# Kernel optimization log

Hardware: AMD Instinct MI355X
Metric: run time of the kernel (lower is better)

Reference implementation:

```python
import jax, jax.numpy as jnp
import numpy as np

D_MODEL = 256
N_HEADS = 8
D_HEAD = D_MODEL // N_HEADS
EMB = [16, 16, 16, 16]
CUMSUM = [0, 16, 32, 48, 64]
PSUM = sum(EMB)
LEVELS = [(122, 122), (61, 61), (31, 31), (16, 16)]
S_TOTAL = sum(h * w for h, w in LEVELS)
IMG = 976.0


def swap_pairs(x):
    # swap consecutive pairs along the leading (view) dim
    return x.reshape(-1, 2, *x.shape[1:])[:, ::-1].reshape(x.shape)


def grid_sample_bilinear(img, grid):
    # img: [B, H, W, D]; grid: [B, Q, 2] in [-1, 1]; align_corners=False, zero padding
    B, H, W, D = img.shape
    gx = (grid[..., 0] + 1.0) * (W * 0.5) - 0.5
    gy = (grid[..., 1] + 1.0) * (H * 0.5) - 0.5
    x0 = jnp.floor(gx)
    y0 = jnp.floor(gy)
    wx = (gx - x0)[..., None]
    wy = (gy - y0)[..., None]
    x0i = x0.astype(jnp.int32)
    y0i = y0.astype(jnp.int32)
    flat = img.reshape(B, H * W, D)

    def gather(xi, yi):
        valid = ((xi >= 0) & (xi < W) & (yi >= 0) & (yi < H)).astype(img.dtype)
        idx = jnp.clip(yi, 0, H - 1) * W + jnp.clip(xi, 0, W - 1)
        v = jnp.take_along_axis(flat, idx[..., None], axis=1)
        return v * valid[..., None]

    v00 = gather(x0i, y0i)
    v01 = gather(x0i + 1, y0i)
    v10 = gather(x0i, y0i + 1)
    v11 = gather(x0i + 1, y0i + 1)
    return (v00 * (1 - wx) * (1 - wy) + v01 * wx * (1 - wy)
            + v10 * (1 - wx) * wy + v11 * wx * wy)


def ms_deform_attn_core(value, shapes, sampling_locations, attention_weights):
    # value: [N, S, M, D]; sampling_locations: [N, Lq, M, P, 2]; attention_weights: [N, Lq, M, P]
    N, S, M, D = value.shape
    Lq = sampling_locations.shape[1]
    grids = 2.0 * sampling_locations - 1.0
    outs = []
    start = 0
    for lid, (H, W) in enumerate(shapes):
        p0, p1 = CUMSUM[lid], CUMSUM[lid + 1]
        Pl = p1 - p0
        v = value[:, start:start + H * W].reshape(N, H, W, M, D)
        v = v.transpose(0, 3, 1, 2, 4).reshape(N * M, H, W, D)
        g = grids[:, :, :, p0:p1].transpose(0, 2, 1, 3, 4).reshape(N * M, Lq * Pl, 2)
        outs.append(grid_sample_bilinear(v, g).reshape(N * M, Lq, Pl, D))
        start += H * W
    samp = jnp.concatenate(outs, axis=2)  # [N*M, Lq, Psum, D]
    w = attention_weights.transpose(0, 2, 1, 3).reshape(N * M, Lq, PSUM, 1)
    out = (samp * w).sum(axis=2)  # [N*M, Lq, D]
    return out.reshape(N, M, Lq, D).transpose(0, 2, 1, 3).reshape(N, Lq, M * D)


def _forward(query, input_flatten, reference_points, p_pfws, pt_transforms,
             W_val, b_val, W_attn, b_attn, W_out, b_out, shapes):
    N, Lq, _ = query.shape
    value = (input_flatten @ W_val.T + b_val).reshape(N, -1, N_HEADS, D_HEAD)
    attn = jax.nn.softmax((query @ W_attn.T + b_attn).reshape(N, Lq, N_HEADS, PSUM), axis=-1)

    # reverse 2x3 affine transform on reference points, scale to pixels
    A = pt_transforms[:, :, :2]
    t = pt_transforms[:, :, 2]
    orig = jnp.einsum('nij,nqj->nqi', jnp.linalg.inv(A), reference_points - t[:, None, :]) * IMG

    # epipolar line in the second (swapped) view: point(x) = ts + ms * x, x in [0, IMG]
    P1 = p_pfws
    P2 = swap_pairs(p_pfws)
    A1 = P1[:, :, :3]
    b1 = P1[:, :, 3]
    cam = -jnp.linalg.solve(A1, b1[:, :, None])[:, :, 0]  # camera center [N,3]
    uh = jnp.concatenate([orig, jnp.ones_like(orig[..., :1])], -1)
    ray = jnp.einsum('nij,nqj->nqi', jnp.linalg.inv(A1), uh - b1[:, None, :])  # [N,Q,3]

    def proj2(X):
        Xh = jnp.concatenate([X, jnp.ones_like(X[..., :1])], -1)
        y = jnp.einsum('nij,nqj->nqi', P2, Xh)
        return y[..., :2] / (y[..., 2:3] + 1e-8)

    ts = proj2(jnp.broadcast_to(cam[:, None, :], ray.shape))
    ms = (proj2(ray) - ts) / IMG

    locs = []
    for n_pts in EMB:
        xs = jnp.linspace(0.0, IMG, n_pts)
        locs.append(ts[:, :, None, :] + ms[:, :, None, :] * xs[None, None, :, None])
    loc = jnp.concatenate(locs, axis=2) / IMG  # [N, Lq, Psum, 2]

    T2 = swap_pairs(pt_transforms)
    loc = jnp.einsum('nij,nqpj->nqpi', T2[:, :, :2], loc) + T2[:, :, 2][:, None, None, :]
    loc = jnp.clip(loc, 0.0, 1.0)
    samp_loc = jnp.broadcast_to(loc[:, :, None, :, :], (N, Lq, N_HEADS, PSUM, 2))

    out = ms_deform_attn_core(swap_pairs(value), shapes, samp_loc, attn)
    return out @ W_out.T + b_out


def setup_inputs() -> dict:
    key = jax.random.key(0)
    ks = jax.random.split(key, 12)
    N, Lq = 4, 1000
    query = jax.random.normal(ks[0], (N, Lq, D_MODEL), jnp.float32)
    input_flatten = jax.random.normal(ks[1], (N, S_TOTAL, D_MODEL), jnp.float32)
    reference_points = jax.random.uniform(ks[2], (N, Lq, 2), jnp.float32)
    p_pfws = jnp.asarray(np.eye(3, 4), jnp.float32) + 0.05 * jax.random.normal(ks[3], (N, 3, 4), jnp.float32)
    pt_transforms = jnp.asarray(np.eye(2, 3), jnp.float32) + 0.05 * jax.random.normal(ks[4], (N, 2, 3), jnp.float32)
    W_val = 0.05 * jax.random.normal(ks[5], (D_MODEL, D_MODEL), jnp.float32)
    b_val = jnp.zeros((D_MODEL,), jnp.float32)
    W_attn = 0.05 * jax.random.normal(ks[6], (N_HEADS * PSUM, D_MODEL), jnp.float32)
    b_attn = jnp.zeros((N_HEADS * PSUM,), jnp.float32)
    W_out = 0.05 * jax.random.normal(ks[7], (D_MODEL, D_MODEL), jnp.float32)
    b_out = jnp.zeros((D_MODEL,), jnp.float32)
    input_spatial_shapes = np.asarray(LEVELS, np.int64)
    input_level_start_index = np.asarray(np.cumsum([0] + [h * w for h, w in LEVELS])[:-1], np.int64)
    return {"query": query, "input_flatten": input_flatten, "reference_points": reference_points,
            "p_pfws": p_pfws, "pt_transforms": pt_transforms,
            "W_val": W_val, "b_val": b_val, "W_attn": W_attn, "b_attn": b_attn,
            "W_out": W_out, "b_out": b_out,
            "input_spatial_shapes": input_spatial_shapes,
            "input_level_start_index": input_level_start_index}


def reference(query, input_flatten, reference_points, p_pfws, pt_transforms,
              W_val, b_val, W_attn, b_attn, W_out, b_out,
              input_spatial_shapes, input_level_start_index):
    shapes = [(int(h), int(w)) for h, w in np.asarray(input_spatial_shapes)]
    return _forward(query, input_flatten, reference_points, p_pfws, pt_transforms,
                    W_val, b_val, W_attn, b_attn, W_out, b_out, shapes)
```

## Files before the change

### kernel.cpp

```cpp
#include <hip/hip_runtime.h>
#include <hip/hip_bf16.h>
#include <math.h>

#define NB 4
#define LQ 1000
#define NHEAD 8
#define DHEAD 32
#define DMODEL 256
#define PSUM 64
#define STOT 19822
#define IMGF 976.0f
#define GK 256

__device__ __constant__ int c_LH[4] = {122, 61, 31, 16};
__device__ __constant__ int c_LW[4] = {122, 61, 31, 16};
__device__ __constant__ int c_LST[4] = {0, 14884, 18605, 19566};

typedef __attribute__((ext_vector_type(8))) short bf16x8;
typedef __attribute__((ext_vector_type(4))) float f32x4;

__device__ inline unsigned int pk2(float a, float b) {
    unsigned short ua = __bfloat16_as_ushort(__float2bfloat16(a));
    unsigned short ub = __bfloat16_as_ushort(__float2bfloat16(b));
    return (unsigned int)ua | ((unsigned int)ub << 16);
}
__device__ inline float bf2f(unsigned short u) {
    return __uint_as_float(((unsigned int)u) << 16);
}
__device__ inline bf16x8 cvt8(float4 u, float4 v) {
    union { unsigned int w[4]; bf16x8 h; } r;
    r.w[0] = pk2(u.x, u.y); r.w[1] = pk2(u.z, u.w);
    r.w[2] = pk2(v.x, v.y); r.w[3] = pk2(v.z, v.w);
    return r.h;
}
__device__ inline void gll16(const void* g, void* l) {
    __builtin_amdgcn_global_load_lds(
        (const __attribute__((address_space(1))) void*)g,
        (__attribute__((address_space(3))) void*)l, 16, 0, 0);
}
__device__ inline void hard_barrier() {
    asm volatile("" ::: "memory");
    __builtin_amdgcn_sched_barrier(0);
    __builtin_amdgcn_s_barrier();
    __builtin_amdgcn_sched_barrier(0);
    asm volatile("" ::: "memory");
}

__device__ inline void make_consts(int n, const float* p_pfws, const float* pt,
                                   float* consts) {
    const float* P1 = p_pfws + n * 12;
    const float* P2 = p_pfws + (n ^ 1) * 12;
    const float* T  = pt + n * 6;
    const float* T2 = pt + (n ^ 1) * 6;
    float* C = consts + n * 48;
    float det = T[0]*T[4] - T[1]*T[3];
    float idet = 1.0f/det;
    C[0] =  T[4]*idet; C[1] = -T[1]*idet;
    C[2] = -T[3]*idet; C[3] =  T[0]*idet;
    C[4] = T[2]; C[5] = T[5];
    float a=P1[0], b=P1[1], c=P1[2];
    float d=P1[4], e=P1[5], f=P1[6];
    float g=P1[8], h=P1[9], i=P1[10];
    float b10=P1[3], b11=P1[7], b12=P1[11];
    float A_=e*i-f*h, B_=c*h-b*i, Cc=b*f-c*e;
    float D_=f*g-d*i, E_=a*i-c*g, F_=c*d-a*f;
    float G_=d*h-e*g, H_=b*g-a*h, I_=a*e-b*d;
    float det3 = a*A_ + b*D_ + c*G_;
    float id3 = 1.0f/det3;
    C[6]=A_*id3;  C[7]=B_*id3;  C[8]=Cc*id3;
    C[9]=D_*id3;  C[10]=E_*id3; C[11]=F_*id3;
    C[12]=G_*id3; C[13]=H_*id3; C[14]=I_*id3;
    C[15]=b10; C[16]=b11; C[17]=b12;
    for (int k = 0; k < 12; ++k) C[18+k] = P2[k];
    float cam0 = -(C[6]*b10  + C[7]*b11  + C[8]*b12);
    float cam1 = -(C[9]*b10  + C[10]*b11 + C[11]*b12);
    float cam2 = -(C[12]*b10 + C[13]*b11 + C[14]*b12);
    float y0 = P2[0]*cam0 + P2[1]*cam1 + P2[2]*cam2  + P2[3];
    float y1 = P2[4]*cam0 + P2[5]*cam1 + P2[6]*cam2  + P2[7];
    float y2 = P2[8]*cam0 + P2[9]*cam1 + P2[10]*cam2 + P2[11];
    float inv = 1.0f/(y2 + 1e-8f);
    C[30] = y0*inv; C[31] = y1*inv;
    for (int k = 0; k < 6; ++k) C[32+k] = T2[k];
}

__global__ void prep(const float* __restrict__ Wv, const float* __restrict__ Wa,
                     const float* __restrict__ Wo,
                     unsigned short* __restrict__ wbv, unsigned short* __restrict__ wba,
                     unsigned short* __restrict__ wbo,
                     const float* __restrict__ p_pfws, const float* __restrict__ pt,
                     float* __restrict__ consts) {
    int bid = blockIdx.x;
    if (bid == 256) {
        int n = threadIdx.x;
        if (n < NB) make_consts(n, p_pfws, pt, consts);
        return;
    }
    int i = bid * 256 + threadIdx.x;
    const float* src; unsigned short* dst; int off;
    if (i < 16384)      { src = Wv; dst = wbv; off = i; }
    else if (i < 49152) { src = Wa; dst = wba; off = i - 16384; }
    else                { src = Wo; dst = wbo; off = i - 49152; }
    float4 f = ((const float4*)src)[off];
    ushort4 o;
    o.x = __bfloat16_as_ushort(__float2bfloat16(f.x));
    o.y = __bfloat16_as_ushort(__float2bfloat16(f.y));
    o.z = __bfloat16_as_ushort(__float2bfloat16(f.z));
    o.w = __bfloat16_as_ushort(__float2bfloat16(f.w));
    ((ushort4*)dst)[off] = o;
}

__global__ __launch_bounds__(256, 1)
void gemm_val_regB(const float* __restrict__ X, const unsigned short* __restrict__ Wb,
                   const float* __restrict__ bias, unsigned short* __restrict__ out,
                   int M, int T, int CHUNK) {
    __shared__ __align__(16) char As[2][32768];
    const int tid  = threadIdx.x;
    const int lane = tid & 63;
    const int wq   = tid >> 6;
    const int l15  = lane & 15;
    const int koct = lane >> 4;
    const int t0   = blockIdx.x * CHUNK;
    int nt = T - t0; if (nt > CHUNK) nt = CHUNK;
    if (nt <= 0) return;

    bf16x8 breg[8][4];
    #pragma unroll
    for (int ks = 0; ks < 8; ++ks)
        #pragma unroll
        for (int ni = 0; ni < 4; ++ni) {
            int col = wq * 64 + ni * 16 + l15;
            breg[ks][ni] = *(const bf16x8*)((const char*)Wb + (size_t)col * 512
                                            + ks * 64 + koct * 16);
        }
    float bias_v[4];
    #pragma unroll
    for (int ni = 0; ni < 4; ++ni) bias_v[ni] = bias[wq * 64 + ni * 16 + l15];

#define STAGE(g, b) do {                                                      \
        _Pragma("unroll") for (int j = 0; j < 8; ++j) {                       \
            int r_ = wq * 8 + j;                                              \
            int gr_ = (g) * 32 + r_; if (gr_ >= M) gr_ = M - 1;               \
            int lch_ = lane ^ (r_ & 7);                                       \
            gll16(X + (size_t)gr_ * GK + lch_ * 4, As[b] + r_ * 1024);        \
        } } while (0)

    STAGE(t0, 0);
    if (nt > 1) { STAGE(t0 + 1, 1); asm volatile("s_waitcnt vmcnt(8)" ::: "memory"); }
    else        {                   asm volatile("s_waitcnt vmcnt(0)" ::: "memory"); }
    hard_barrier();

#define COMPUTE_STORE(g, b) do {                                              \
        f32x4 acc[2][4] = {};                                                 \
        _Pragma("unroll") for (int ks = 0; ks < 8; ++ks) {                    \
            _Pragma("unroll") for (int mi = 0; mi < 2; ++mi) {                \
                int r_ = mi * 16 + l15;                                       \
                int ch_ = ks * 8 + koct * 2;                                  \
                float4 x0_ = *(const float4*)(As[b] + r_ * 1024 +             \
                                              ((ch_    ) ^ (r_ & 7)) * 16);   \
                float4 x1_ = *(const float4*)(As[b] + r_ * 1024 +             \
                                              ((ch_ + 1) ^ (r_ & 7)) * 16);   \
                bf16x8 af_ = cvt8(x0_, x1_);                                  \
                _Pragma("unroll") for (int ni = 0; ni < 4; ++ni)              \
                    acc[mi][ni] = __builtin_amdgcn_mfma_f32_16x16x32_bf16(    \
                        af_, breg[ks][ni], acc[mi][ni], 0, 0, 0);             \
            }                                                                 \
        }                                                                     \
        _Pragma("unroll") for (int mi = 0; mi < 2; ++mi) {                    \
            int rb_ = (g) * 32 + mi * 16 + (lane >> 4) * 4;                   \
            _Pragma("unroll") for (int j_ = 0; j_ < 4; ++j_) {                \
                int gr_ = rb_ + j_;                                           \
                if (gr_ < M) {                                                \
                    _Pragma("unroll") for (int ni = 0; ni < 4; ++ni)          \
                        out[(size_t)gr_ * DMODEL + wq * 64 + ni * 16 + l15] = \
                            __bfloat16_as_ushort(__float2bfloat16(            \
                                acc[mi][ni][j_] + bias_v[ni]));               \
                }                                                             \
            }                                                                 \
        } } while (0)

    for (int t = 0; t < nt; ++t) {
        COMPUTE_STORE(t0 + t, t & 1);
        if (t + 1 == nt) break;
        hard_barrier();
        if (t + 2 < nt) {
            STAGE(t0 + t + 2, t & 1);
            asm volatile("s_waitcnt vmcnt(40)" ::: "memory");
        } else {
            asm volatile("s_waitcnt vmcnt(32)" ::: "memory");
        }
        hard_barrier();
    }
#undef COMPUTE_STORE
#undef STAGE
}

template<bool OUT_BF16>
__global__ __launch_bounds__(256, 4)
void gemm64(const float* __restrict__ A, const unsigned short* __restrict__ Bb,
            const float* __restrict__ bias, void* __restrict__ outp,
            int M, int N) {
    __shared__ char smem[40960];
    char* asmem = smem;
    char* bsmem = smem + 8192;
    const int tid  = threadIdx.x;
    const int lane = tid & 63;
    const int w    = tid >> 6;
    const int l15  = lane & 15;
    const int koct = lane >> 4;
    const int i0 = blockIdx.x * 64;
    const int o0 = blockIdx.y * 256;

    const int s_row = tid >> 2;
    const int s_q   = tid & 3;
    int gr = i0 + s_row; gr = gr < M ? gr : M - 1;
    const float* aptr = A + (size_t)gr * GK + s_q * 16;
    const int s_sw = (s_row & 7) << 4;
    char* a_w0 = asmem + s_row * 128 + ((s_q * 32)      ^ s_sw);
    char* a_w1 = asmem + s_row * 128 + ((s_q * 32 + 16) ^ s_sw);

    const int b_sub = lane >> 3;
    const int b_kc  = (lane & 7) ^ b_sub;

    f32x4 acc[4][4] = {};
    float bias_v[4];
    #pragma unroll
    for (int ni = 0; ni < 4; ++ni) bias_v[ni] = bias[o0 + w * 64 + ni * 16 + l15];

    for (int t = 0; t < 4; ++t) {
        const int k0 = t * 64;
        #pragma unroll
        for (int j = 0; j < 8; ++j) {
            int cI = w * 8 + j;
            int col = cI * 8 + b_sub;
            gll16(Bb + (size_t)(o0 + col) * GK + k0 + b_kc * 8,
                  bsmem + cI * 1024);
        }
        {
            const float4* s = (const float4*)(aptr + k0);
            float4 f0 = s[0], f1 = s[1], f2 = s[2], f3 = s[3];
            uint4 wv0, wv1;
            wv0.x = pk2(f0.x,f0.y); wv0.y = pk2(f0.z,f0.w);
            wv0.z = pk2(f1.x,f1.y); wv0.w = pk2(f1.z,f1.w);
            wv1.x = pk2(f2.x,f2.y); wv1.y = pk2(f2.z,f2.w);
            wv1.z = pk2(f3.x,f3.y); wv1.w = pk2(f3.z,f3.w);
            *(uint4*)a_w0 = wv0;
            *(uint4*)a_w1 = wv1;
        }
        __syncthreads();
        #pragma unroll
        for (int ks = 0; ks < 2; ++ks) {
            const int kc = ks * 4 + koct;
            bf16x8 af[4], bfr[4];
            #pragma unroll
            for (int mi = 0; mi < 4; ++mi) {
                int r = mi * 16 + l15;
                af[mi] = *(const bf16x8*)(asmem + r * 128 + ((kc * 16) ^ ((r & 7) << 4)));
            }
            #pragma unroll
            for (int ni = 0; ni < 4; ++ni) {
                int c = w * 64 + ni * 16 + l15;
                bfr[ni] = *(const bf16x8*)(bsmem + c * 128 + ((kc * 16) ^ ((c & 7) << 4)));
            }
            #pragma unroll
            for (int mi = 0; mi < 4; ++mi)
                #pragma unroll
                for (int ni = 0; ni < 4; ++ni)
                    acc[mi][ni] = __builtin_amdgcn_mfma_f32_16x16x32_bf16(
                        af[mi], bfr[ni], acc[mi][ni], 0, 0, 0);
        }
        __syncthreads();
    }

    #pragma unroll
    for (int mi = 0; mi < 4; ++mi) {
        int rbase = i0 + mi * 16 + (lane >> 4) * 4;
        #pragma unroll
        for (int j = 0; j < 4; ++j) {
            int grow = rbase + j;
            if (grow < M) {
                #pragma unroll
                for (int ni = 0; ni < 4; ++ni) {
                    int gcol = o0 + w * 64 + ni * 16 + l15;
                    float v = acc[mi][ni][j] + bias_v[ni];
                    if (OUT_BF16)
                        ((unsigned short*)outp)[(size_t)grow * N + gcol] =
                            __bfloat16_as_ushort(__float2bfloat16(v));
                    else
                        ((float*)outp)[(size_t)grow * N + gcol] = v;
                }
            }
        }
    }
}

__global__ __launch_bounds__(256)
void fused_sample(const float* __restrict__ logits,
                  const float* __restrict__ ref_pts,
                  const unsigned short* __restrict__ value,
                  const float* __restrict__ consts,
                  float* __restrict__ attn_out) {
    int b = blockIdx.x;
    int n = b / LQ;
    int q = b - n * LQ;
    int tid = threadIdx.x;

    __shared__ float s_attn[512];
    __shared__ float s_loc[16][2];
    __shared__ int   s_idx[64][4];
    __shared__ float s_w[64][4];
    __shared__ float4 s_part[4][64];

    s_attn[tid]       = logits[(size_t)b * 512 + tid];
    s_attn[tid + 256] = logits[(size_t)b * 512 + tid + 256];
    __syncthreads();

    {
        int wave = tid >> 6, lane = tid & 63;
        for (int h = wave; h < NHEAD; h += 4) {
            float v = s_attn[h * 64 + lane];
            float mx = v;
            #pragma unroll
            for (int off = 32; off; off >>= 1) mx = fmaxf(mx, __shfl_xor(mx, off, 64));
            float e = expf(v - mx);
            float sm = e;
            #pragma unroll
            for (int off = 32; off; off >>= 1) sm += __shfl_xor(sm, off, 64);
            s_attn[h * 64 + lane] = e / sm;
        }
    }

    if (tid < 16) {
        const float* C = consts + n * 48;
        float rx = ref_pts[((size_t)n * LQ + q) * 2 + 0];
        float ry = ref_pts[((size_t)n * LQ + q) * 2 + 1];
        float dx = rx - C[4], dy = ry - C[5];
        float ox = (C[0]*dx + C[1]*dy) * IMGF;
        float oy = (C[2]*dx + C[3]*dy) * IMGF;
        float u0 = ox - C[15], u1 = oy - C[16], u2 = 1.0f - C[17];
        float r0 = C[6]*u0  + C[7]*u1  + C[8]*u2;
        float r1 = C[9]*u0  + C[10]*u1 + C[11]*u2;
        float r2 = C[12]*u0 + C[13]*u1 + C[14]*u2;
        float y0 = C[18]*r0 + C[19]*r1 + C[20]*r2 + C[21];
        float y1 = C[22]*r0 + C[23]*r1 + C[24]*r2 + C[25];
        float y2 = C[26]*r0 + C[27]*r1 + C[28]*r2 + C[29];
        float inv = 1.0f/(y2 + 1e-8f);
        float prx = y0*inv, pry = y1*inv;
        float ts0 = C[30], ts1 = C[31];
        float msx = (prx - ts0) / IMGF, msy = (pry - ts1) / IMGF;
        int j = tid;
        float xsj = IMGF * ((float)j / 15.0f);
        float lx = (ts0 + msx * xsj) / IMGF;
        float ly = (ts1 + msy * xsj) / IMGF;
        float Lx = C[32]*lx + C[33]*ly + C[34];
        float Ly = C[35]*lx + C[36]*ly + C[37];
        s_loc[j][0] = fminf(fmaxf(Lx, 0.0f), 1.0f);
        s_loc[j][1] = fminf(fmaxf(Ly, 0.0f), 1.0f);
    }
    __syncthreads();

    if (tid < 64) {
        int p = tid, lev = p >> 4, j = p & 15;
        int H = c_LH[lev], W = c_LW[lev], st = c_LST[lev];
        float gx = s_loc[j][0] * (float)W - 0.5f;
        float gy = s_loc[j][1] * (float)H - 0.5f;
        float x0f = floorf(gx), y0f = floorf(gy);
        float wx = gx - x0f, wy = gy - y0f;
        int x0 = (int)x0f, y0 = (int)y0f;
        int x1 = x0 + 1, y1 = y0 + 1;
        bool vx0 = (x0 >= 0) & (x0 < W), vx1 = (x1 >= 0) & (x1 < W);
        bool vy0 = (y0 >= 0) & (y0 < H), vy1 = (y1 >= 0) & (y1 < H);
        s_idx[p][0] = (vx0 & vy0) ? st + y0 * W + x0 : -1;  s_w[p][0] = (1.f-wx)*(1.f-wy);
        s_idx[p][1] = (vx1 & vy0) ? st + y0 * W + x1 : -1;  s_w[p][1] = wx*(1.f-wy);
        s_idx[p][2] = (vx0 & vy1) ? st + y1 * W + x0 : -1;  s_w[p][2] = (1.f-wx)*wy;
        s_idx[p][3] = (vx1 & vy1) ? st + y1 * W + x1 : -1;  s_w[p][3] = wx*wy;
    }
    __syncthreads();

    int wv = tid >> 6, lane = tid & 63;
    const unsigned short* vbase = value + (size_t)(n ^ 1) * STOT * DMODEL + lane * 4;
    int m = lane >> 3;
    float a0 = 0.f, a1 = 0.f, a2 = 0.f, a3 = 0.f;
    #pragma unroll 8
    for (int j = 0; j < 16; ++j) {
        int p = wv * 16 + j;
        float wa = s_attn[m * 64 + p];
        float s0 = 0.f, s1 = 0.f, s2 = 0.f, s3 = 0.f;
        #pragma unroll
        for (int cc = 0; cc < 4; ++cc) {
            int idx = s_idx[p][cc];
            if (idx >= 0) {
                ushort4 vv = *(const ushort4*)(vbase + (size_t)idx * DMODEL);
                float wgt = s_w[p][cc];
                s0 += wgt * bf2f(vv.x);
                s1 += wgt * bf2f(vv.y);
                s2 += wgt * bf2f(vv.z);
                s3 += wgt * bf2f(vv.w);
            }
        }
        a0 += wa * s0; a1 += wa * s1; a2 += wa * s2; a3 += wa * s3;
    }
    s_part[wv][lane] = make_float4(a0, a1, a2, a3);
    __syncthreads();

    const float* sp = (const float*)s_part;
    float r = sp[tid] + sp[256 + tid] + sp[512 + tid] + sp[768 + tid];
    attn_out[(size_t)b * DMODEL + tid] = r;
}

extern "C" void kernel_launch(void* const* d_in, const int* in_sizes, int n_in,
                              void* d_out, int out_size, void* d_ws, size_t ws_size,
                              hipStream_t stream) {
    const float* query         = (const float*)d_in[0];
    const float* input_flatten = (const float*)d_in[1];
    const float* ref_pts       = (const float*)d_in[2];
    const float* p_pfws        = (const float*)d_in[3];
    const float* pt            = (const float*)d_in[4];
    const float* W_val         = (const float*)d_in[5];
    const float* b_val         = (const float*)d_in[6];
    const float* W_attn        = (const float*)d_in[7];
    const float* b_attn        = (const float*)d_in[8];
    const float* W_out         = (const float*)d_in[9];
    const float* b_out         = (const float*)d_in[10];
    float* out = (float*)d_out;

    const int M = NB * STOT;
    const size_t value_bytes  = (size_t)M * DMODEL * 2;
    const size_t logits_bytes = (size_t)NB * LQ * 512 * 4;
    const size_t attn_bytes   = (size_t)NB * LQ * DMODEL * 4;
    const size_t consts_bytes = NB * 48 * 4;
    const size_t wv_bytes     = (size_t)DMODEL * DMODEL * 2;
    const size_t wa_bytes     = (size_t)512 * DMODEL * 2;
    const size_t wo_bytes     = (size_t)DMODEL * DMODEL * 2;
    const size_t need = value_bytes + logits_bytes + attn_bytes + consts_bytes
                      + wv_bytes + wa_bytes + wo_bytes;
    if (ws_size < need) return;

    char* p = (char*)d_ws;
    unsigned short* value = (unsigned short*)p;  p += value_bytes;
    float* logits   = (float*)p;                 p += logits_bytes;
    float* attn_out = (float*)p;                 p += attn_bytes;
    float* consts   = (float*)p;                 p += consts_bytes;
    unsigned short* wb_val  = (unsigned short*)p; p += wv_bytes;
    unsigned short* wb_attn = (unsigned short*)p; p += wa_bytes;
    unsigned short* wb_out  = (unsigned short*)p; p += wo_bytes;

    prep<<<257, 256, 0, stream>>>(W_val, W_attn, W_out, wb_val, wb_attn, wb_out,
                                  p_pfws, pt, consts);

    {
        const int T = (M + 31) / 32;
        const int CHUNK = 5;
        const int blocks = (T + CHUNK - 1) / CHUNK;
        gemm_val_regB<<<blocks, 256, 0, stream>>>(input_flatten, wb_val, b_val,
                                                  value, M, T, CHUNK);
    }
    {
        dim3 g((NB * LQ + 63) / 64, 2);
        gemm64<false><<<g, 256, 0, stream>>>(query, wb_attn, b_attn, logits, NB * LQ, 512);
    }
    fused_sample<<<NB * LQ, 256, 0, stream>>>(logits, ref_pts, value, consts, attn_out);
    {
        dim3 g((NB * LQ + 63) / 64, 1);
        gemm64<false><<<g, 256, 0, stream>>>(attn_out, wb_out, b_out, out, NB * LQ, DMODEL);
    }
}
```

Measured before the change: 100.00 us.

## Widen fused_sample to 512 threads with 16-byte gathers and clamped indices

```diff
diff --git a/kernel.cpp b/kernel.cpp
--- a/kernel.cpp
+++ b/kernel.cpp
@@ -293,7 +293,7 @@
     }
 }
 
-__global__ __launch_bounds__(256)
+__global__ __launch_bounds__(512)
 void fused_sample(const float* __restrict__ logits,
                   const float* __restrict__ ref_pts,
                   const unsigned short* __restrict__ value,
@@ -308,25 +308,23 @@
     __shared__ float s_loc[16][2];
     __shared__ int   s_idx[64][4];
     __shared__ float s_w[64][4];
-    __shared__ float4 s_part[4][64];
-
-    s_attn[tid]       = logits[(size_t)b * 512 + tid];
-    s_attn[tid + 256] = logits[(size_t)b * 512 + tid + 256];
+    __shared__ float s_part[8][32][9];
+
+    s_attn[tid] = logits[(size_t)b * 512 + tid];
     __syncthreads();
 
     {
         int wave = tid >> 6, lane = tid & 63;
-        for (int h = wave; h < NHEAD; h += 4) {
-            float v = s_attn[h * 64 + lane];
-            float mx = v;
-            #pragma unroll
-            for (int off = 32; off; off >>= 1) mx = fmaxf(mx, __shfl_xor(mx, off, 64));
-            float e = expf(v - mx);
-            float sm = e;
-            #pragma unroll
-            for (int off = 32; off; off >>= 1) sm += __shfl_xor(sm, off, 64);
-            s_attn[h * 64 + lane] = e / sm;
-        }
+        float v = s_attn[wave * 64 + lane];
+        float mx = v;
+        #pragma unroll
+        for (int off = 32; off; off >>= 1) mx = fmaxf(mx, __shfl_xor(mx, off, 64));
+        float e = expf(v - mx);
+        float sm = e;
+        #pragma unroll
+        for (int off = 32; off; off >>= 1) sm += __shfl_xor(sm, off, 64);
+        __syncthreads();
+        s_attn[wave * 64 + lane] = e / sm;
     }
 
     if (tid < 16) {
@@ -369,42 +367,62 @@
         int x1 = x0 + 1, y1 = y0 + 1;
         bool vx0 = (x0 >= 0) & (x0 < W), vx1 = (x1 >= 0) & (x1 < W);
         bool vy0 = (y0 >= 0) & (y0 < H), vy1 = (y1 >= 0) & (y1 < H);
-        s_idx[p][0] = (vx0 & vy0) ? st + y0 * W + x0 : -1;  s_w[p][0] = (1.f-wx)*(1.f-wy);
-        s_idx[p][1] = (vx1 & vy0) ? st + y0 * W + x1 : -1;  s_w[p][1] = wx*(1.f-wy);
-        s_idx[p][2] = (vx0 & vy1) ? st + y1 * W + x0 : -1;  s_w[p][2] = (1.f-wx)*wy;
-        s_idx[p][3] = (vx1 & vy1) ? st + y1 * W + x1 : -1;  s_w[p][3] = wx*wy;
+        int x0c = min(max(x0, 0), W - 1), x1c = min(max(x1, 0), W - 1);
+        int y0c = min(max(y0, 0), H - 1), y1c = min(max(y1, 0), H - 1);
+        s_idx[p][0] = st + y0c * W + x0c;  s_w[p][0] = (vx0 & vy0) ? (1.f-wx)*(1.f-wy) : 0.f;
+        s_idx[p][1] = st + y0c * W + x1c;  s_w[p][1] = (vx1 & vy0) ? wx*(1.f-wy)       : 0.f;
+        s_idx[p][2] = st + y1c * W + x0c;  s_w[p][2] = (vx0 & vy1) ? (1.f-wx)*wy       : 0.f;
+        s_idx[p][3] = st + y1c * W + x1c;  s_w[p][3] = (vx1 & vy1) ? wx*wy             : 0.f;
     }
     __syncthreads();
 
     int wv = tid >> 6, lane = tid & 63;
-    const unsigned short* vbase = value + (size_t)(n ^ 1) * STOT * DMODEL + lane * 4;
-    int m = lane >> 3;
-    float a0 = 0.f, a1 = 0.f, a2 = 0.f, a3 = 0.f;
-    #pragma unroll 8
-    for (int j = 0; j < 16; ++j) {
-        int p = wv * 16 + j;
+    int half = lane >> 5, l31 = lane & 31;
+    const unsigned short* valb = value + (size_t)(n ^ 1) * STOT * DMODEL + l31 * 8;
+    int m = l31 >> 2;
+    float a0=0.f,a1=0.f,a2=0.f,a3=0.f,a4=0.f,a5=0.f,a6=0.f,a7=0.f;
+    #pragma unroll
+    for (int j = 0; j < 4; ++j) {
+        int p = wv * 8 + j * 2 + half;
         float wa = s_attn[m * 64 + p];
-        float s0 = 0.f, s1 = 0.f, s2 = 0.f, s3 = 0.f;
-        #pragma unroll
-        for (int cc = 0; cc < 4; ++cc) {
-            int idx = s_idx[p][cc];
-            if (idx >= 0) {
-                ushort4 vv = *(const ushort4*)(vbase + (size_t)idx * DMODEL);
-                float wgt = s_w[p][cc];
-                s0 += wgt * bf2f(vv.x);
-                s1 += wgt * bf2f(vv.y);
-                s2 += wgt * bf2f(vv.z);
-                s3 += wgt * bf2f(vv.w);
+        bf16x8 v0 = *(const bf16x8*)(valb + (size_t)s_idx[p][0] * DMODEL);
+        bf16x8 v1 = *(const bf16x8*)(valb + (size_t)s_idx[p][1] * DMODEL);
+        bf16x8 v2 = *(const bf16x8*)(valb + (size_t)s_idx[p][2] * DMODEL);
+        bf16x8 v3 = *(const bf16x8*)(valb + (size_t)s_idx[p][3] * DMODEL);
+        float w0 = s_w[p][0], w1 = s_w[p][1], w2 = s_w[p][2], w3 = s_w[p][3];
+        #pragma unroll
+        for (int e = 0; e < 8; ++e) {
+            float s = w0 * bf2f((unsigned short)v0[e]) + w1 * bf2f((unsigned short)v1[e])
+                    + w2 * bf2f((unsigned short)v2[e]) + w3 * bf2f((unsigned short)v3[e]);
+            float ws = wa * s;
+            switch (e) {
+                case 0: a0 += ws; break; case 1: a1 += ws; break;
+                case 2: a2 += ws; break; case 3: a3 += ws; break;
+                case 4: a4 += ws; break; case 5: a5 += ws; break;
+                case 6: a6 += ws; break; case 7: a7 += ws; break;
             }
         }
-        a0 += wa * s0; a1 += wa * s1; a2 += wa * s2; a3 += wa * s3;
-    }
-    s_part[wv][lane] = make_float4(a0, a1, a2, a3);
+    }
+    a0 += __shfl_xor(a0, 32, 64);  a1 += __shfl_xor(a1, 32, 64);
+    a2 += __shfl_xor(a2, 32, 64);  a3 += __shfl_xor(a3, 32, 64);
+    a4 += __shfl_xor(a4, 32, 64);  a5 += __shfl_xor(a5, 32, 64);
+    a6 += __shfl_xor(a6, 32, 64);  a7 += __shfl_xor(a7, 32, 64);
+    if (half == 0) {
+        s_part[wv][l31][0] = a0; s_part[wv][l31][1] = a1;
+        s_part[wv][l31][2] = a2; s_part[wv][l31][3] = a3;
+        s_part[wv][l31][4] = a4; s_part[wv][l31][5] = a5;
+        s_part[wv][l31][6] = a6; s_part[wv][l31][7] = a7;
+    }
     __syncthreads();
 
-    const float* sp = (const float*)s_part;
-    float r = sp[tid] + sp[256 + tid] + sp[512 + tid] + sp[768 + tid];
-    attn_out[(size_t)b * DMODEL + tid] = r;
+    if (tid < DMODEL) {
+        int cg = tid >> 3, ce = tid & 7;
+        float r = s_part[0][cg][ce] + s_part[1][cg][ce]
+                + s_part[2][cg][ce] + s_part[3][cg][ce]
+                + s_part[4][cg][ce] + s_part[5][cg][ce]
+                + s_part[6][cg][ce] + s_part[7][cg][ce];
+        attn_out[(size_t)b * DMODEL + tid] = r;
+    }
 }
 
 extern "C" void kernel_launch(void* const* d_in, const int* in_sizes, int n_in,
@@ -458,7 +476,7 @@
         dim3 g((NB * LQ + 63) / 64, 2);
         gemm64<false><<<g, 256, 0, stream>>>(query, wb_attn, b_attn, logits, NB * LQ, 512);
     }
-    fused_sample<<<NB * LQ, 256, 0, stream>>>(logits, ref_pts, value, consts, attn_out);
+    fused_sample<<<NB * LQ, 512, 0, stream>>>(logits, ref_pts, value, consts, attn_out);
     {
         dim3 g((NB * LQ + 63) / 64, 1);
         gemm64<false><<<g, 256, 0, stream>>>(attn_out, wb_out, b_out, out, NB * LQ, DMODEL);
```

After: 112.0 us. 12.0% more time.
